# Performance work log

Measured on AMD Instinct MI355X. Metric: run time of the kernel, lower is better.

The kernel has to match this reference:

```python
import jax, jax.numpy as jnp
import numpy as np

B, T, D, H, L = 8, 64, 128, 4, 4
G = B * T            # 512 frame-graphs
NPG = 200            # nodes per graph
N = G * NPG          # 102400 nodes
E = 8 * N            # 819200 edges
FIN, HID = 2, 64
DH = D // H
NCLS = 2


def setup_inputs():
    key = jax.random.key(0)
    ks = jax.random.split(key, 16)
    w = lambda k, s: (jax.random.normal(k, s) * 0.05).astype(jnp.float32)
    x = jax.random.normal(ks[0], (N, FIN), dtype=jnp.float32)
    g = jax.random.randint(ks[1], (E,), 0, G)
    src = (g * NPG + jax.random.randint(ks[2], (E,), 0, NPG)).astype(jnp.int32)
    dst = (g * NPG + jax.random.randint(ks[3], (E,), 0, NPG)).astype(jnp.int32)
    node_graph = (jnp.arange(N) // NPG).astype(jnp.int32)
    return dict(
        x=x, edge_src=src, edge_dst=dst, node_graph=node_graph,
        gW1=w(ks[4], (FIN, HID)), gb1=jnp.zeros((HID,), jnp.float32),
        ln1g=jnp.ones((HID,), jnp.float32), ln1b=jnp.zeros((HID,), jnp.float32),
        gW2=w(ks[5], (HID, HID)), gb2=jnp.zeros((HID,), jnp.float32),
        ln2g=jnp.ones((HID,), jnp.float32), ln2b=jnp.zeros((HID,), jnp.float32),
        gW3=w(ks[6], (HID, D)), gb3=jnp.zeros((D,), jnp.float32),
        tWqkv=w(ks[7], (L, 3 * D, D)), tbqkv=jnp.zeros((L, 3 * D), jnp.float32),
        tWo=w(ks[8], (L, D, D)), tbo=jnp.zeros((L, D), jnp.float32),
        tg1=jnp.ones((L, D), jnp.float32), tb1=jnp.zeros((L, D), jnp.float32),
        tg2=jnp.ones((L, D), jnp.float32), tb2=jnp.zeros((L, D), jnp.float32),
        tWf1=w(ks[9], (L, 4 * D, D)), tbf1=jnp.zeros((L, 4 * D), jnp.float32),
        tWf2=w(ks[10], (L, D, 4 * D)), tbf2=jnp.zeros((L, D), jnp.float32),
        hW1=w(ks[11], (D // 2, D)), hb1=jnp.zeros((D // 2,), jnp.float32),
        hW2=w(ks[12], (NCLS, D // 2)), hb2=jnp.zeros((NCLS,), jnp.float32),
    )


def _ln(x, g, b, eps=1e-5):
    m = jnp.mean(x, -1, keepdims=True)
    v = jnp.var(x, -1, keepdims=True)
    return (x - m) * jax.lax.rsqrt(v + eps) * g + b


def _forward(x, edge_src, edge_dst, node_graph, gW1, gb1, ln1g, ln1b, gW2, gb2,
             ln2g, ln2b, gW3, gb3, tWqkv, tbqkv, tWo, tbo, tg1, tb1, tg2, tb2,
             tWf1, tbf1, tWf2, tbf2, hW1, hb1, hW2, hb2):
    # --- GCN encoder (PyG GCNConv: sym-normalized A with self loops) ---
    loops = jnp.arange(N, dtype=jnp.int32)
    src = jnp.concatenate([edge_src, loops])
    dst = jnp.concatenate([edge_dst, loops])
    deg = jnp.zeros((N,), x.dtype).at[dst].add(1.0)
    dinv = jax.lax.rsqrt(deg)
    norm = (dinv[src] * dinv[dst])[:, None]

    def gcn(h, W, b):
        h = h @ W  # transform first (smaller message dim when FIN < HID)
        return jax.ops.segment_sum(h[src] * norm, dst, num_segments=N) + b

    h = _ln(jax.nn.relu(gcn(x, gW1, gb1)), ln1g, ln1b)
    h = _ln(jax.nn.relu(gcn(h, gW2, gb2)), ln2g, ln2b)
    h = gcn(h, gW3, gb3)  # (N, D)

    # per-graph mean readout (replaces the python loop in the original)
    cnt = jax.ops.segment_sum(jnp.ones((N,), h.dtype), node_graph, num_segments=G)
    emb = jax.ops.segment_sum(h, node_graph, num_segments=G) / cnt[:, None]
    seq = emb.reshape(B, T, D)

    # --- sinusoidal positional encoding ---
    pos = jnp.arange(T, dtype=jnp.float32)[:, None]
    div = jnp.exp(jnp.arange(0, D, 2, dtype=jnp.float32) * (-np.log(10000.0) / D))
    pe = jnp.zeros((T, D), jnp.float32)
    pe = pe.at[:, 0::2].set(jnp.sin(pos * div)).at[:, 1::2].set(jnp.cos(pos * div))
    seq = seq + pe

    # --- TransformerEncoder (post-norm, relu FFN, batch_first) ---
    scale = 1.0 / np.sqrt(DH)
    for l in range(L):
        qkv = seq @ tWqkv[l].T + tbqkv[l]
        q, k, v = jnp.split(qkv, 3, axis=-1)
        q = q.reshape(B, T, H, DH).transpose(0, 2, 1, 3)
        k = k.reshape(B, T, H, DH).transpose(0, 2, 1, 3)
        v = v.reshape(B, T, H, DH).transpose(0, 2, 1, 3)
        att = jax.nn.softmax(jnp.einsum('bhqd,bhkd->bhqk', q, k) * scale, axis=-1)
        a = jnp.einsum('bhqk,bhkd->bhqd', att, v).transpose(0, 2, 1, 3).reshape(B, T, D)
        seq = _ln(seq + a @ tWo[l].T + tbo[l], tg1[l], tb1[l])
        f = jax.nn.relu(seq @ tWf1[l].T + tbf1[l]) @ tWf2[l].T + tbf2[l]
        seq = _ln(seq + f, tg2[l], tb2[l])

    pooled = jnp.mean(seq, axis=1)  # mask=None path -> plain temporal mean
    return jax.nn.relu(pooled @ hW1.T + hb1) @ hW2.T + hb2  # (B, NCLS)


def reference(x, edge_src, edge_dst, node_graph, gW1, gb1, ln1g, ln1b, gW2, gb2,
              ln2g, ln2b, gW3, gb3, tWqkv, tbqkv, tWo, tbo, tg1, tb1, tg2, tb2,
              tWf1, tbf1, tWf2, tbf2, hW1, hb1, hW2, hb2):
    return _forward(x, edge_src, edge_dst, node_graph, gW1, gb1, ln1g, ln1b,
                    gW2, gb2, ln2g, ln2b, gW3, gb3, tWqkv, tbqkv, tWo, tbo,
                    tg1, tb1, tg2, tb2, tWf1, tbf1, tWf2, tbf2, hW1, hb1, hW2, hb2)
```

## Files before the change

kernel.cpp:

```cpp
#include <hip/hip_runtime.h>

#define NN   102400
#define EE   819200
#define GG   512
#define NPG  200
#define DD   128
#define TT   64
#define BB   8
#define LL   4
#define NB_A   320
#define ECH_A  2560
#define SCAP 2560
#define NSLOT 16
#define CHK  50

typedef unsigned int uint;

static __device__ __forceinline__ void wave_sum64_2(float& a, float& b) {
#pragma unroll
    for (int off = 32; off > 0; off >>= 1) {
        a += __shfl_xor(a, off, 64);
        b += __shfl_xor(b, off, 64);
    }
}


__global__ __launch_bounds__(256) void k_a1(const int* __restrict__ src,
                                            int* __restrict__ hist) {
    __shared__ int h[GG];
    int tid = threadIdx.x;
    h[tid] = 0; h[tid + 256] = 0;
    __syncthreads();
    int base = blockIdx.x * ECH_A;
#pragma unroll
    for (int it = 0; it < ECH_A / 256; ++it)
        atomicAdd(&h[src[base + it * 256 + tid] / NPG], 1);
    __syncthreads();
    hist[blockIdx.x * GG + tid] = h[tid];
    hist[blockIdx.x * GG + tid + 256] = h[tid + 256];
}

__global__ __launch_bounds__(64) void k_a2a(const int* __restrict__ hist,
                                            int* __restrict__ gcnt) {
    int g = blockIdx.x, lane = threadIdx.x;
    int s = 0;
#pragma unroll
    for (int i = 0; i < NB_A / 64; ++i) s += hist[(i * 64 + lane) * GG + g];
#pragma unroll
    for (int off = 32; off > 0; off >>= 1) s += __shfl_xor(s, off, 64);
    if (lane == 0) gcnt[g] = s;
}

__global__ __launch_bounds__(512) void k_a2b(const int* __restrict__ gcnt,
                                             int* __restrict__ goff) {
    __shared__ int sm[GG];
    int g = threadIdx.x;
    int c = gcnt[g];
    sm[g] = c;
    __syncthreads();
    for (int d = 1; d < GG; d <<= 1) {
        int v = (g >= d) ? sm[g - d] : 0;
        __syncthreads();
        sm[g] += v;
        __syncthreads();
    }
    goff[g] = sm[g] - c;
    if (g == GG - 1) goff[GG] = sm[g];
}

__global__ __launch_bounds__(512) void k_a2c(const int* __restrict__ hist,
                                             const int* __restrict__ goff,
                                             int* __restrict__ off2) {
    int g = blockIdx.x * 8 + (threadIdx.x >> 6);
    int lane = threadIdx.x & 63;
    int running = goff[g];
#pragma unroll
    for (int cchunk = 0; cchunk < NB_A / 64; ++cchunk) {
        int b = cchunk * 64 + lane;
        int v = hist[b * GG + g];
        int s = v;
#pragma unroll
        for (int off = 1; off < 64; off <<= 1) {
            int t_ = __shfl_up(s, off, 64);
            if (lane >= off) s += t_;
        }
        off2[b * GG + g] = running + s - v;
        running += __shfl(s, 63, 64);
    }
}

__global__ __launch_bounds__(256) void k_a3(const int* __restrict__ src,
                                            const int* __restrict__ dst,
                                            const int* __restrict__ off2,
                                            uint* __restrict__ gpack) {
    __shared__ int cur[GG];
    int tid = threadIdx.x;
    cur[tid] = off2[blockIdx.x * GG + tid];
    cur[tid + 256] = off2[blockIdx.x * GG + tid + 256];
    __syncthreads();
    int base = blockIdx.x * ECH_A;
#pragma unroll
    for (int it = 0; it < ECH_A / 256; ++it) {
        int e = base + it * 256 + tid;
        int s = src[e], d = dst[e];
        int g = s / NPG;
        int pos = atomicAdd(&cur[g], 1);
        gpack[pos] = ((uint)(s - g * NPG) << 8) | (uint)(d - g * NPG);
    }
}

__global__ __launch_bounds__(256) void k_bsort(
    const float* __restrict__ x, const int* __restrict__ goff,
    const uint* __restrict__ gpack, const float* __restrict__ W1,
    const float* __restrict__ gb1, const float* __restrict__ lng,
    const float* __restrict__ lnb, uint2* __restrict__ slots,
    uint2* __restrict__ ovf, int* __restrict__ ovfcnt,
    float* __restrict__ wgtv, float* __restrict__ hout) {
    int g = ((blockIdx.x & 7) << 6) | (blockIdx.x >> 3);
    __shared__ float2 xs[NPG];
    __shared__ float2 aggl[NPG];
    __shared__ int cnt2[NPG];
    __shared__ int lnoff[NPG + 1];
    __shared__ int cur[NPG];
    __shared__ float rsq[NPG];
    __shared__ float cwl[NPG];
    __shared__ uint srec[SCAP];
    __shared__ int sm[256];
    __shared__ uint2 ovfl[128];
    __shared__ int ovfcur;
    int tid = threadIdx.x;
    int base = goff[g], E = goff[g + 1] - base;
    const float2* x2 = (const float2*)x;
    if (tid < NPG) { xs[tid] = x2[g * NPG + tid]; cnt2[tid] = 0; cwl[tid] = 0.f; }
    if (tid == 0) ovfcur = 0;
    __syncthreads();
    for (int i = tid; i < E; i += 256) atomicAdd(&cnt2[gpack[base + i] & 255u], 1);
    __syncthreads();
    int c = (tid < NPG) ? cnt2[tid] : 0;
    sm[tid] = c;
    __syncthreads();
    for (int d = 1; d < 256; d <<= 1) {
        int v = (tid >= d) ? sm[tid - d] : 0;
        __syncthreads();
        sm[tid] += v;
        __syncthreads();
    }
    if (tid < NPG) {
        lnoff[tid] = sm[tid] - c;
        cur[tid] = sm[tid] - c;
        rsq[tid] = rsqrtf((float)(c + 1));
    }
    if (tid == 0) lnoff[NPG] = E;
    __syncthreads();
    for (int i = tid; i < E; i += 256) {
        uint r = gpack[base + i];
        int pos = atomicAdd(&cur[r & 255u], 1);
        srec[pos] = r;
    }
    __syncthreads();
    for (int i = tid; i < E; i += 256) {
        uint r = srec[i];
        atomicAdd(&cwl[r >> 8], rsq[r >> 8] * rsq[r & 255u]);
    }
    __syncthreads();
    {
        uint2* sbase = &slots[(size_t)g * NPG * NSLOT];
        for (int li = tid; li < NPG * NSLOT; li += 256) {
            int n = li >> 4, s = li & 15;
            int e0 = lnoff[n];
            int En = lnoff[n + 1] - e0;
            float rd = rsq[n];
            uint2 v;
            if (s == 0) {
                v = make_uint2((uint)(g * NPG + n), __float_as_uint(rd * rd));
            } else if (s - 1 < En) {
                uint r = srec[e0 + s - 1];
                int ls = (int)(r >> 8);
                v = make_uint2((uint)(g * NPG + ls), __float_as_uint(rsq[ls] * rd));
            } else {
                v = make_uint2((uint)(g * NPG + n), 0u);
            }
            sbase[li] = v;
        }
    }
    if (tid < NPG) {
        float rd = rsq[tid];
        float dv = rd * rd;
        float ax = xs[tid].x * dv, ay = xs[tid].y * dv;
        int e0 = lnoff[tid], e1 = lnoff[tid + 1];
        for (int e = e0; e < e1; ++e) {
            uint r = srec[e];
            int ls = (int)(r >> 8);
            float w = rsq[ls] * rd;
            ax += xs[ls].x * w;
            ay += xs[ls].y * w;
        }
        for (int e = e0 + NSLOT - 1; e < e1; ++e) {
            uint r = srec[e];
            int ls = (int)(r >> 8);
            int p = atomicAdd(&ovfcur, 1);
            if (p < 128)
                ovfl[p] = make_uint2(((uint)tid << 17) | (uint)(g * NPG + ls),
                                     __float_as_uint(rsq[ls] * rd));
        }
        aggl[tid] = make_float2(ax, ay);
        wgtv[g * NPG + tid] = cwl[tid] + dv;
    }
    __syncthreads();
    int nov = ovfcur < 128 ? ovfcur : 128;
    if (tid == 0) ovfcnt[g] = nov;
    if (tid < nov) ovf[g * 128 + tid] = ovfl[tid];
    int lane = tid & 63, wid = tid >> 6;
    float w0 = W1[lane], w1 = W1[64 + lane];
    float gbj = gb1[lane], lgj = lng[lane], lbj = lnb[lane];
    for (int i = wid; i < NPG; i += 4) {
        float2 a = aggl[i];
        float u = fmaxf(a.x * w0 + a.y * w1 + gbj, 0.f);
        float s2 = u, q2 = u * u;
        wave_sum64_2(s2, q2);
        float mean = s2 * (1.f / 64.f);
        float var = q2 * (1.f / 64.f) - mean * mean;
        hout[(size_t)(g * NPG + i) * 64 + lane] = (u - mean) * rsqrtf(var + 1e-5f) * lgj + lbj;
    }
}


__global__ __launch_bounds__(256) void k_agg_lin_pool(
    const float* __restrict__ t, const float* __restrict__ W,
    const float* __restrict__ gb, const float* __restrict__ lng,
    const float* __restrict__ lnb, const uint2* __restrict__ slots,
    const uint2* __restrict__ ovf, const int* __restrict__ ovfcnt,
    const float* __restrict__ wgtv, float* __restrict__ pooled) {
    int c = ((blockIdx.x & 7) << 8) | (blockIdx.x >> 3);
    int n0 = c * CHK;
    int g = c >> 2, lbase = (c & 3) * CHK;
    __shared__ float hs[CHK][64];
    __shared__ uint2 slt[CHK][NSLOT];
    __shared__ float wgt[CHK];
    __shared__ float red[4][64];
    int tid = threadIdx.x, lane = tid & 63, wid = tid >> 6;
    int grp = lane >> 4, fq = lane & 15;
    {
        const float4* s4 = (const float4*)&slots[(size_t)n0 * NSLOT];
        float4* d4 = (float4*)slt;
        for (int i = tid; i < CHK * NSLOT / 2; i += 256) d4[i] = s4[i];
    }
    if (tid < CHK) wgt[tid] = wgtv[n0 + tid];
    __syncthreads();
    for (int i = wid; i < CHK; i += 4) {
        float4 acc = make_float4(0.f, 0.f, 0.f, 0.f);
#pragma unroll
        for (int r = 0; r < 4; ++r) {
            uint2 s = slt[i][r * 4 + grp];
            float w = __uint_as_float(s.y);
            float4 tv = *(const float4*)&t[(size_t)s.x * 64 + fq * 4];
            acc.x += tv.x * w; acc.y += tv.y * w;
            acc.z += tv.z * w; acc.w += tv.w * w;
        }
        acc.x += __shfl_xor(acc.x, 16); acc.y += __shfl_xor(acc.y, 16);
        acc.z += __shfl_xor(acc.z, 16); acc.w += __shfl_xor(acc.w, 16);
        acc.x += __shfl_xor(acc.x, 32); acc.y += __shfl_xor(acc.y, 32);
        acc.z += __shfl_xor(acc.z, 32); acc.w += __shfl_xor(acc.w, 32);
        if (grp == 0) *(float4*)&hs[i][fq * 4] = acc;
    }
    __syncthreads();
    int nov = ovfcnt[g];
    if (nov && wid == 0) {
        for (int k = 0; k < nov; ++k) {
            uint2 r = ovf[g * 128 + k];
            int ld = r.x >> 17;
            if (ld >= lbase && ld < lbase + CHK)
                hs[ld - lbase][lane] +=
                    t[(size_t)(r.x & 0x1FFFFu) * 64 + lane] * __uint_as_float(r.y);
        }
    }
    __syncthreads();
    float wreg[64];
#pragma unroll
    for (int k = 0; k < 64; ++k) wreg[k] = W[k * 64 + lane];
    float gbj = gb[lane], lgj = lng[lane], lbj = lnb[lane];
    float psum = 0.f;
    for (int i = wid; i < CHK; i += 4) {
        const float4* hrow = (const float4*)&hs[i][0];
        float a0 = 0.f, a1 = 0.f;
#pragma unroll
        for (int k4 = 0; k4 < 16; k4 += 2) {
            float4 h0 = hrow[k4], h1 = hrow[k4 + 1];
            a0 += h0.x * wreg[4 * k4] + h0.y * wreg[4 * k4 + 1] +
                  h0.z * wreg[4 * k4 + 2] + h0.w * wreg[4 * k4 + 3];
            a1 += h1.x * wreg[4 * k4 + 4] + h1.y * wreg[4 * k4 + 5] +
                  h1.z * wreg[4 * k4 + 6] + h1.w * wreg[4 * k4 + 7];
        }
        float u = fmaxf(a0 + a1 + gbj, 0.f);
        float s = u, q = u * u;
        wave_sum64_2(s, q);
        float mean = s * (1.f / 64.f);
        float var = q * (1.f / 64.f) - mean * mean;
        float h = (u - mean) * rsqrtf(var + 1e-5f) * lgj + lbj;
        psum += h * wgt[i];
    }
    red[wid][lane] = psum;
    __syncthreads();
    if (tid < 64)
        atomicAdd(&pooled[g * 64 + tid],
                  red[0][tid] + red[1][tid] + red[2][tid] + red[3][tid]);
}

__global__ __launch_bounds__(128) void k_emb(
    const float* __restrict__ pooled, const float* __restrict__ W3,
    const float* __restrict__ b3, float* __restrict__ seq) {
    int g = blockIdx.x, d = threadIdx.x;
    __shared__ float ps[64];
    if (d < 64) ps[d] = pooled[g * 64 + d] * (1.f / NPG);
    __syncthreads();
    float a = b3[d];
#pragma unroll 8
    for (int k = 0; k < 64; ++k) a += ps[k] * W3[k * DD + d];
    float freq = expf((float)(d & ~1) * (-9.210340371976184f / 128.f));
    float ang = (float)(g & (TT - 1)) * freq;
    a += (d & 1) ? cosf(ang) : sinf(ang);
    seq[(size_t)g * DD + d] = a;
}


__global__ __launch_bounds__(512) void k_qkv_attn(
    const float* __restrict__ seq, const float* __restrict__ Wqkv,
    const float* __restrict__ bqkv, float* __restrict__ abuf) {
    int b = blockIdx.x >> 2, h = blockIdx.x & 3;
    __shared__ float seqs[64][132];
    __shared__ float Qs[64][36], Ks[64][36], Vs[64][36];
    __shared__ float Ss[64][68];
    int tid = threadIdx.x;
    for (int i = tid; i < 64 * 32; i += 512) {
        int r = i >> 5, c = i & 31;
        float4 v = *(const float4*)&seq[(size_t)(b * 64 + r) * DD + c * 4];
        *(float4*)&seqs[r][c * 4] = v;
    }
    __syncthreads();
    {
        int r = tid & 63, jg = tid >> 6;
        float acc[12];
        int wrow[12];
#pragma unroll
        for (int i = 0; i < 12; ++i) {
            int jj = jg * 12 + i;
            int row = (jj < 32) ? (h * 32 + jj)
                    : (jj < 64) ? (128 + h * 32 + jj - 32)
                                : (256 + h * 32 + jj - 64);
            wrow[i] = row;
            acc[i] = bqkv[row];
        }
        for (int kc = 0; kc < 8; ++kc) {
            float4 s0 = *(const float4*)&seqs[r][kc * 16 + 0];
            float4 s1 = *(const float4*)&seqs[r][kc * 16 + 4];
            float4 s2 = *(const float4*)&seqs[r][kc * 16 + 8];
            float4 s3 = *(const float4*)&seqs[r][kc * 16 + 12];
#pragma unroll
            for (int i = 0; i < 12; ++i) {
                const float4* wp = (const float4*)&Wqkv[(size_t)wrow[i] * DD + kc * 16];
                float4 w0 = wp[0], w1 = wp[1], w2 = wp[2], w3 = wp[3];
                acc[i] += s0.x * w0.x + s0.y * w0.y + s0.z * w0.z + s0.w * w0.w +
                          s1.x * w1.x + s1.y * w1.y + s1.z * w1.z + s1.w * w1.w +
                          s2.x * w2.x + s2.y * w2.y + s2.z * w2.z + s2.w * w2.w +
                          s3.x * w3.x + s3.y * w3.y + s3.z * w3.z + s3.w * w3.w;
            }
        }
#pragma unroll
        for (int i = 0; i < 12; ++i) {
            int jj = jg * 12 + i;
            if (jj < 32) Qs[r][jj] = acc[i];
            else if (jj < 64) Ks[r][jj - 32] = acc[i];
            else Vs[r][jj - 64] = acc[i];
        }
    }
    __syncthreads();
    int q = tid >> 3, kg = tid & 7;
    const float scale = 0.17677669529663687f;
    float p[8];
    float mx = -1e30f;
#pragma unroll
    for (int kk = 0; kk < 8; ++kk) {
        int k = kg * 8 + kk;
        float a = 0.f;
#pragma unroll
        for (int dq = 0; dq < 8; ++dq) {
            float4 qv = *(const float4*)&Qs[q][dq * 4];
            float4 kv = *(const float4*)&Ks[k][dq * 4];
            a += qv.x * kv.x + qv.y * kv.y + qv.z * kv.z + qv.w * kv.w;
        }
        p[kk] = a * scale;
        mx = fmaxf(mx, p[kk]);
    }
    mx = fmaxf(mx, __shfl_xor(mx, 1));
    mx = fmaxf(mx, __shfl_xor(mx, 2));
    mx = fmaxf(mx, __shfl_xor(mx, 4));
    float ssum = 0.f;
#pragma unroll
    for (int kk = 0; kk < 8; ++kk) {
        p[kk] = expf(p[kk] - mx);
        ssum += p[kk];
    }
    ssum += __shfl_xor(ssum, 1);
    ssum += __shfl_xor(ssum, 2);
    ssum += __shfl_xor(ssum, 4);
    float inv = 1.f / ssum;
#pragma unroll
    for (int kk = 0; kk < 8; ++kk) Ss[q][kg * 8 + kk] = p[kk] * inv;
    __syncthreads();
    float4 o = make_float4(0.f, 0.f, 0.f, 0.f);
    for (int k = 0; k < 64; ++k) {
        float pw = Ss[q][k];
        float4 v = *(const float4*)&Vs[k][kg * 4];
        o.x += pw * v.x; o.y += pw * v.y; o.z += pw * v.z; o.w += pw * v.w;
    }
    *(float4*)&abuf[(size_t)(b * 64 + q) * DD + h * 32 + kg * 4] = o;
}

__global__ __launch_bounds__(256) void k_post(
    const float* __restrict__ abuf, const float* __restrict__ Wo,
    const float* __restrict__ bo, const float* __restrict__ g1,
    const float* __restrict__ bl1, const float* __restrict__ Wf1,
    const float* __restrict__ bf1, const float* __restrict__ Wf2,
    const float* __restrict__ bf2, const float* __restrict__ g2,
    const float* __restrict__ bl2, float* __restrict__ seq) {
    int m0 = blockIdx.x * 2, tid = threadIdx.x;
    __shared__ float arow[2][128];
    __shared__ float srow[2][128];
    __shared__ float f1[2][512];
    __shared__ float pf[2][128];
    __shared__ float sred[4][2];
    __shared__ float sred2[2][4];
    int rr = tid >> 7, d0 = tid & 127;
    arow[rr][d0] = abuf[(size_t)(m0 + rr) * DD + d0];
    __syncthreads();
    {
        float acc = bo[d0];
        const float4* wr = (const float4*)&Wo[(size_t)d0 * DD];
        const float4* ar = (const float4*)arow[rr];
#pragma unroll
        for (int k = 0; k < 32; ++k) {
            float4 w = wr[k], a = ar[k];
            acc += a.x * w.x + a.y * w.y + a.z * w.z + a.w * w.w;
        }
        float u = seq[(size_t)(m0 + rr) * DD + d0] + acc;
        float s = u, q = u * u;
        wave_sum64_2(s, q);
        int wv = tid >> 6;
        if ((tid & 63) == 0) { sred[wv][0] = s; sred[wv][1] = q; }
        __syncthreads();
        int wp = rr * 2;
        s = sred[wp][0] + sred[wp + 1][0];
        q = sred[wp][1] + sred[wp + 1][1];
        float mean = s * (1.f / 128.f);
        float var = q * (1.f / 128.f) - mean * mean;
        float rstd = rsqrtf(var + 1e-5f);
        srow[rr][d0] = (u - mean) * rstd * g1[d0] + bl1[d0];
    }
    __syncthreads();
    const float4* s0 = (const float4*)srow[0];
    const float4* s1 = (const float4*)srow[1];
#pragma unroll
    for (int rep = 0; rep < 2; ++rep) {
        int o = tid + rep * 256;
        float bv = bf1[o];
        float a0 = bv, a1 = bv;
        const float4* wr = (const float4*)&Wf1[(size_t)o * DD];
#pragma unroll
        for (int k = 0; k < 32; ++k) {
            float4 w = wr[k];
            float4 x0 = s0[k], x1 = s1[k];
            a0 += x0.x * w.x + x0.y * w.y + x0.z * w.z + x0.w * w.w;
            a1 += x1.x * w.x + x1.y * w.y + x1.z * w.z + x1.w * w.w;
        }
        f1[0][o] = fmaxf(a0, 0.f);
        f1[1][o] = fmaxf(a1, 0.f);
    }
    __syncthreads();
    int d = tid & 127, half = tid >> 7;
    float b0 = half ? 0.f : bf2[d];
    float a0 = b0, a1 = b0;
    const float4* wr2 = (const float4*)&Wf2[(size_t)d * 512 + half * 256];
    const float4* f10 = (const float4*)&f1[0][half * 256];
    const float4* f11 = (const float4*)&f1[1][half * 256];
#pragma unroll
    for (int k = 0; k < 64; ++k) {
        float4 w = wr2[k];
        float4 x0 = f10[k], x1 = f11[k];
        a0 += x0.x * w.x + x0.y * w.y + x0.z * w.z + x0.w * w.w;
        a1 += x1.x * w.x + x1.y * w.y + x1.z * w.z + x1.w * w.w;
    }
    if (half) { pf[0][d] = a0; pf[1][d] = a1; }
    __syncthreads();
    if (half == 0) {
        float u0 = srow[0][d] + a0 + pf[0][d];
        float u1 = srow[1][d] + a1 + pf[1][d];
        float s0_ = u0, q0_ = u0 * u0, s1_ = u1, q1_ = u1 * u1;
        wave_sum64_2(s0_, q0_);
        wave_sum64_2(s1_, q1_);
        int w_ = d >> 6;
        if ((d & 63) == 0) {
            sred2[w_][0] = s0_; sred2[w_][1] = q0_;
            sred2[w_][2] = s1_; sred2[w_][3] = q1_;
        }
        __syncthreads();
        float S0 = sred2[0][0] + sred2[1][0], Q0 = sred2[0][1] + sred2[1][1];
        float S1 = sred2[0][2] + sred2[1][2], Q1 = sred2[0][3] + sred2[1][3];
        float mean0 = S0 * (1.f / 128.f);
        float var0 = Q0 * (1.f / 128.f) - mean0 * mean0;
        float rstd0 = rsqrtf(var0 + 1e-5f);
        float mean1 = S1 * (1.f / 128.f);
        float var1 = Q1 * (1.f / 128.f) - mean1 * mean1;
        float rstd1 = rsqrtf(var1 + 1e-5f);
        seq[(size_t)m0 * DD + d] = (u0 - mean0) * rstd0 * g2[d] + bl2[d];
        seq[(size_t)(m0 + 1) * DD + d] = (u1 - mean1) * rstd1 * g2[d] + bl2[d];
    } else {
        __syncthreads();
    }
}

__global__ __launch_bounds__(128) void k_head(
    const float* __restrict__ seq, const float* __restrict__ W1,
    const float* __restrict__ b1, const float* __restrict__ W2,
    const float* __restrict__ b2, float* __restrict__ out) {
    int b = blockIdx.x, t = threadIdx.x;
    __shared__ float pooled[DD];
    __shared__ float hid[64];
    float s = 0.f;
    for (int i = 0; i < TT; ++i) s += seq[(size_t)(b * TT + i) * DD + t];
    pooled[t] = s * (1.f / TT);
    __syncthreads();
    if (t < 64) {
        float a = b1[t];
        const float* wr = W1 + t * DD;
        for (int k = 0; k < DD; ++k) a += pooled[k] * wr[k];
        hid[t] = fmaxf(a, 0.f);
    }
    __syncthreads();
    if (t < 2) {
        float a = b2[t];
        const float* wr = W2 + t * 64;
        for (int k = 0; k < 64; ++k) a += hid[k] * wr[k];
        out[b * 2 + t] = a;
    }
}


extern "C" void kernel_launch(void* const* d_in, const int* in_sizes, int n_in,
                              void* d_out, int out_size, void* d_ws, size_t ws_size,
                              hipStream_t stream) {
    const float* x     = (const float*)d_in[0];
    const int*   esrc  = (const int*)d_in[1];
    const int*   edst  = (const int*)d_in[2];
    const float* gW1   = (const float*)d_in[4];
    const float* gb1   = (const float*)d_in[5];
    const float* ln1g  = (const float*)d_in[6];
    const float* ln1b  = (const float*)d_in[7];
    const float* gW2   = (const float*)d_in[8];
    const float* gb2   = (const float*)d_in[9];
    const float* ln2g  = (const float*)d_in[10];
    const float* ln2b  = (const float*)d_in[11];
    const float* gW3   = (const float*)d_in[12];
    const float* gb3   = (const float*)d_in[13];
    const float* tWqkv = (const float*)d_in[14];
    const float* tbqkv = (const float*)d_in[15];
    const float* tWo   = (const float*)d_in[16];
    const float* tbo   = (const float*)d_in[17];
    const float* tg1   = (const float*)d_in[18];
    const float* tb1   = (const float*)d_in[19];
    const float* tg2   = (const float*)d_in[20];
    const float* tb2   = (const float*)d_in[21];
    const float* tWf1  = (const float*)d_in[22];
    const float* tbf1  = (const float*)d_in[23];
    const float* tWf2  = (const float*)d_in[24];
    const float* tbf2  = (const float*)d_in[25];
    const float* hW1   = (const float*)d_in[26];
    const float* hb1   = (const float*)d_in[27];
    const float* hW2   = (const float*)d_in[28];
    const float* hb2   = (const float*)d_in[29];
    float* out = (float*)d_out;

    int*   hist   = (int*)d_ws;
    int*   off2   = hist + NB_A * GG;
    int*   gcnt   = off2 + NB_A * GG;
    int*   goff   = gcnt + GG;
    uint*  gpack  = (uint*)(goff + 516);
    uint2* slots  = (uint2*)(gpack + EE);
    uint2* ovf    = slots + (size_t)NN * NSLOT;
    int*   ovfcnt = (int*)(ovf + GG * 128);
    float* wgtv   = (float*)(ovfcnt + GG);
    float* pooled = wgtv + NN;
    float* bufA = pooled + GG * 64;
    float* seq  = bufA + (size_t)NN * 64;
    float* abuf = seq + GG * DD;

    hipMemsetAsync(pooled, 0, GG * 64 * sizeof(float), stream);
    k_a1<<<NB_A, 256, 0, stream>>>(esrc, hist);
    k_a2a<<<GG, 64, 0, stream>>>(hist, gcnt);
    k_a2b<<<1, 512, 0, stream>>>(gcnt, goff);
    k_a2c<<<64, 512, 0, stream>>>(hist, goff, off2);
    k_a3<<<NB_A, 256, 0, stream>>>(esrc, edst, off2, gpack);
    k_bsort<<<GG, 256, 0, stream>>>(x, goff, gpack, gW1, gb1, ln1g, ln1b,
                                    slots, ovf, ovfcnt, wgtv, bufA);

    k_agg_lin_pool<<<NN / CHK, 256, 0, stream>>>(bufA, gW2, gb2, ln2g, ln2b,
                                                 slots, ovf, ovfcnt, wgtv, pooled);
    k_emb<<<GG, DD, 0, stream>>>(pooled, gW3, gb3, seq);

    for (int l = 0; l < LL; l++) {
        k_qkv_attn<<<BB * 4, 512, 0, stream>>>(
            seq, tWqkv + (size_t)l * 384 * 128, tbqkv + l * 384, abuf);
        k_post<<<GG / 2, 256, 0, stream>>>(
            abuf, tWo + (size_t)l * 128 * 128, tbo + l * 128,
            tg1 + l * 128, tb1 + l * 128,
            tWf1 + (size_t)l * 512 * 128, tbf1 + l * 512,
            tWf2 + (size_t)l * 128 * 512, tbf2 + l * 128,
            tg2 + l * 128, tb2 + l * 128, seq);
    }

    k_head<<<BB, DD, 0, stream>>>(seq, hW1, hb1, hW2, hb2, out);
}
```

Before: 368.6 us.

## Split fused QKV+attention into separate wide-grid kernels and hoist weight loads

The fused QKV-projection plus attention kernel ran on only 32 blocks. It is split into a per-row QKV projection kernel with 512 blocks and an attention kernel with 128 blocks, each handling 16 queries of one head. The QKV results now go through a new global buffer. In the aggregation kernel, the W register preload moves ahead of the gather phase so its latency overlaps, and the gather loop is unrolled by 2. The trade-off is an extra launch per layer and a global round-trip for QKV, in exchange for far more parallelism on the GPU.

```diff
diff --git a/kernel.cpp b/kernel.cpp
--- a/kernel.cpp
+++ b/kernel.cpp
@@ -240,6 +240,9 @@
     __shared__ float red[4][64];
     int tid = threadIdx.x, lane = tid & 63, wid = tid >> 6;
     int grp = lane >> 4, fq = lane & 15;
+    float wreg[64];
+#pragma unroll
+    for (int k = 0; k < 64; ++k) wreg[k] = W[k * 64 + lane];
     {
         const float4* s4 = (const float4*)&slots[(size_t)n0 * NSLOT];
         float4* d4 = (float4*)slt;
@@ -247,6 +250,7 @@
     }
     if (tid < CHK) wgt[tid] = wgtv[n0 + tid];
     __syncthreads();
+#pragma unroll 2
     for (int i = wid; i < CHK; i += 4) {
         float4 acc = make_float4(0.f, 0.f, 0.f, 0.f);
 #pragma unroll
@@ -275,9 +279,6 @@
         }
     }
     __syncthreads();
-    float wreg[64];
-#pragma unroll
-    for (int k = 0; k < 64; ++k) wreg[k] = W[k * 64 + lane];
     float gbj = gb[lane], lgj = lng[lane], lbj = lnb[lane];
     float psum = 0.f;
     for (int i = wid; i < CHK; i += 4) {
@@ -323,97 +324,99 @@
 }
 
 
-__global__ __launch_bounds__(512) void k_qkv_attn(
+__global__ __launch_bounds__(128) void k_qkv(
     const float* __restrict__ seq, const float* __restrict__ Wqkv,
-    const float* __restrict__ bqkv, float* __restrict__ abuf) {
-    int b = blockIdx.x >> 2, h = blockIdx.x & 3;
-    __shared__ float seqs[64][132];
-    __shared__ float Qs[64][36], Ks[64][36], Vs[64][36];
-    __shared__ float Ss[64][68];
+    const float* __restrict__ bqkv, float* __restrict__ qkvb) {
+    int m = blockIdx.x, tid = threadIdx.x;
+    __shared__ float row[128];
+    row[tid] = seq[(size_t)m * DD + tid];
+    __syncthreads();
+    const float4* r4 = (const float4*)row;
+    float acc0 = bqkv[tid], acc1 = bqkv[tid + 128], acc2 = bqkv[tid + 256];
+    const float4* w0 = (const float4*)&Wqkv[(size_t)tid * DD];
+    const float4* w1 = (const float4*)&Wqkv[(size_t)(tid + 128) * DD];
+    const float4* w2 = (const float4*)&Wqkv[(size_t)(tid + 256) * DD];
+#pragma unroll
+    for (int k = 0; k < 32; ++k) {
+        float4 a = r4[k];
+        float4 x0 = w0[k], x1 = w1[k], x2 = w2[k];
+        acc0 += a.x * x0.x + a.y * x0.y + a.z * x0.z + a.w * x0.w;
+        acc1 += a.x * x1.x + a.y * x1.y + a.z * x1.z + a.w * x1.w;
+        acc2 += a.x * x2.x + a.y * x2.y + a.z * x2.z + a.w * x2.w;
+    }
+    float* ob = qkvb + (size_t)m * 384;
+    ob[tid] = acc0;
+    ob[tid + 128] = acc1;
+    ob[tid + 256] = acc2;
+}
+
+__global__ __launch_bounds__(256) void k_attn(const float* __restrict__ qkvb,
+                                              float* __restrict__ abuf) {
+    int bh = blockIdx.x >> 2, quad = blockIdx.x & 3;
+    int b = bh >> 2, h = bh & 3;
+    __shared__ float Ks[64][36], Vs[64][36];
+    __shared__ float Ss[16][68];
     int tid = threadIdx.x;
-    for (int i = tid; i < 64 * 32; i += 512) {
-        int r = i >> 5, c = i & 31;
-        float4 v = *(const float4*)&seq[(size_t)(b * 64 + r) * DD + c * 4];
-        *(float4*)&seqs[r][c * 4] = v;
-    }
-    __syncthreads();
+    const float* base = qkvb + (size_t)(b * 64) * 384 + h * 32;
+    for (int li = tid; li < 512; li += 256) {
+        int r = li >> 3, cc = li & 7;
+        *(float4*)&Ks[r][cc * 4] = *(const float4*)&base[(size_t)r * 384 + 128 + cc * 4];
+        *(float4*)&Vs[r][cc * 4] = *(const float4*)&base[(size_t)r * 384 + 256 + cc * 4];
+    }
+    __syncthreads();
+    int ql = tid >> 4, kl = tid & 15;
+    int q = quad * 16 + ql;
+    float qreg[32];
     {
-        int r = tid & 63, jg = tid >> 6;
-        float acc[12];
-        int wrow[12];
-#pragma unroll
-        for (int i = 0; i < 12; ++i) {
-            int jj = jg * 12 + i;
-            int row = (jj < 32) ? (h * 32 + jj)
-                    : (jj < 64) ? (128 + h * 32 + jj - 32)
-                                : (256 + h * 32 + jj - 64);
-            wrow[i] = row;
-            acc[i] = bqkv[row];
-        }
-        for (int kc = 0; kc < 8; ++kc) {
-            float4 s0 = *(const float4*)&seqs[r][kc * 16 + 0];
-            float4 s1 = *(const float4*)&seqs[r][kc * 16 + 4];
-            float4 s2 = *(const float4*)&seqs[r][kc * 16 + 8];
-            float4 s3 = *(const float4*)&seqs[r][kc * 16 + 12];
-#pragma unroll
-            for (int i = 0; i < 12; ++i) {
-                const float4* wp = (const float4*)&Wqkv[(size_t)wrow[i] * DD + kc * 16];
-                float4 w0 = wp[0], w1 = wp[1], w2 = wp[2], w3 = wp[3];
-                acc[i] += s0.x * w0.x + s0.y * w0.y + s0.z * w0.z + s0.w * w0.w +
-                          s1.x * w1.x + s1.y * w1.y + s1.z * w1.z + s1.w * w1.w +
-                          s2.x * w2.x + s2.y * w2.y + s2.z * w2.z + s2.w * w2.w +
-                          s3.x * w3.x + s3.y * w3.y + s3.z * w3.z + s3.w * w3.w;
-            }
-        }
-#pragma unroll
-        for (int i = 0; i < 12; ++i) {
-            int jj = jg * 12 + i;
-            if (jj < 32) Qs[r][jj] = acc[i];
-            else if (jj < 64) Ks[r][jj - 32] = acc[i];
-            else Vs[r][jj - 64] = acc[i];
-        }
-    }
-    __syncthreads();
-    int q = tid >> 3, kg = tid & 7;
+        const float4* qp = (const float4*)&base[(size_t)q * 384];
+#pragma unroll
+        for (int i = 0; i < 8; ++i) {
+            float4 v = qp[i];
+            qreg[i * 4] = v.x; qreg[i * 4 + 1] = v.y;
+            qreg[i * 4 + 2] = v.z; qreg[i * 4 + 3] = v.w;
+        }
+    }
     const float scale = 0.17677669529663687f;
-    float p[8];
+    float p[4];
     float mx = -1e30f;
 #pragma unroll
-    for (int kk = 0; kk < 8; ++kk) {
-        int k = kg * 8 + kk;
+    for (int kk = 0; kk < 4; ++kk) {
+        int k = kl * 4 + kk;
         float a = 0.f;
 #pragma unroll
-        for (int dq = 0; dq < 8; ++dq) {
-            float4 qv = *(const float4*)&Qs[q][dq * 4];
-            float4 kv = *(const float4*)&Ks[k][dq * 4];
-            a += qv.x * kv.x + qv.y * kv.y + qv.z * kv.z + qv.w * kv.w;
-        }
+        for (int d = 0; d < 32; ++d) a += qreg[d] * Ks[k][d];
         p[kk] = a * scale;
         mx = fmaxf(mx, p[kk]);
     }
     mx = fmaxf(mx, __shfl_xor(mx, 1));
     mx = fmaxf(mx, __shfl_xor(mx, 2));
     mx = fmaxf(mx, __shfl_xor(mx, 4));
+    mx = fmaxf(mx, __shfl_xor(mx, 8));
     float ssum = 0.f;
 #pragma unroll
-    for (int kk = 0; kk < 8; ++kk) {
+    for (int kk = 0; kk < 4; ++kk) {
         p[kk] = expf(p[kk] - mx);
         ssum += p[kk];
     }
     ssum += __shfl_xor(ssum, 1);
     ssum += __shfl_xor(ssum, 2);
     ssum += __shfl_xor(ssum, 4);
+    ssum += __shfl_xor(ssum, 8);
     float inv = 1.f / ssum;
 #pragma unroll
-    for (int kk = 0; kk < 8; ++kk) Ss[q][kg * 8 + kk] = p[kk] * inv;
-    __syncthreads();
-    float4 o = make_float4(0.f, 0.f, 0.f, 0.f);
+    for (int kk = 0; kk < 4; ++kk) Ss[ql][kl * 4 + kk] = p[kk] * inv;
+    __syncthreads();
+    int d0 = kl * 2;
+    float o0 = 0.f, o1 = 0.f;
+#pragma unroll 4
     for (int k = 0; k < 64; ++k) {
-        float pw = Ss[q][k];
-        float4 v = *(const float4*)&Vs[k][kg * 4];
-        o.x += pw * v.x; o.y += pw * v.y; o.z += pw * v.z; o.w += pw * v.w;
-    }
-    *(float4*)&abuf[(size_t)(b * 64 + q) * DD + h * 32 + kg * 4] = o;
+        float pw = Ss[ql][k];
+        o0 += pw * Vs[k][d0];
+        o1 += pw * Vs[k][d0 + 1];
+    }
+    float* op = abuf + (size_t)(b * 64 + q) * DD + h * 32 + d0;
+    op[0] = o0;
+    op[1] = o1;
 }
 
 __global__ __launch_bounds__(256) void k_post(
@@ -591,7 +594,8 @@
     float* pooled = wgtv + NN;
     float* bufA = pooled + GG * 64;
     float* seq  = bufA + (size_t)NN * 64;
-    float* abuf = seq + GG * DD;
+    float* qkvb = seq + GG * DD;
+    float* abuf = qkvb + GG * 384;
 
     hipMemsetAsync(pooled, 0, GG * 64 * sizeof(float), stream);
     k_a1<<<NB_A, 256, 0, stream>>>(esrc, hist);
@@ -607,8 +611,9 @@
     k_emb<<<GG, DD, 0, stream>>>(pooled, gW3, gb3, seq);
 
     for (int l = 0; l < LL; l++) {
-        k_qkv_attn<<<BB * 4, 512, 0, stream>>>(
-            seq, tWqkv + (size_t)l * 384 * 128, tbqkv + l * 384, abuf);
+        k_qkv<<<GG, 128, 0, stream>>>(
+            seq, tWqkv + (size_t)l * 384 * 128, tbqkv + l * 384, qkvb);
+        k_attn<<<BB * 4 * 4, 256, 0, stream>>>(qkvb, abuf);
         k_post<<<GG / 2, 256, 0, stream>>>(
             abuf, tWo + (size_t)l * 128 * 128, tbo + l * 128,
             tg1 + l * 128, tb1 + l * 128,
```

New measurement: 331.3 us. 10.1% less time.
